# Performance work log

Hardware: AMD Instinct MI355X
Metric: run time of the kernel (lower is better)

Reference implementation:

```python
import jax, jax.numpy as jnp
import numpy as np

B, S, E, H = 2, 2048, 1024, 16
D = E // H  # head_dim = 64


def setup_inputs() -> dict:
    key = jax.random.key(0)
    ks = jax.random.split(key, 14)
    inp = {
        "query": jax.random.normal(ks[0], (B, S, E), jnp.float32),
        "key": jax.random.normal(ks[1], (B, S, E), jnp.float32),
        "value": jax.random.normal(ks[2], (B, S, E), jnp.float32),
        "adj": jax.random.normal(ks[3], (S, S), jnp.float32),
        "mask": jax.random.randint(ks[4], (B, 1, S, S), 0, 2, jnp.int32),
    }
    sc = 1.0 / np.sqrt(E)
    inp["Wq"] = jax.random.normal(ks[5], (E, E), jnp.float32) * sc
    inp["bq"] = jax.random.normal(ks[6], (E,), jnp.float32) * sc
    inp["Wk"] = jax.random.normal(ks[7], (E, E), jnp.float32) * sc
    inp["bk"] = jax.random.normal(ks[8], (E,), jnp.float32) * sc
    inp["Wv"] = jax.random.normal(ks[9], (E, E), jnp.float32) * sc
    inp["bv"] = jax.random.normal(ks[10], (E,), jnp.float32) * sc
    inp["Wo"] = jax.random.normal(ks[11], (E, E), jnp.float32) * sc
    inp["bo"] = jax.random.normal(ks[12], (E,), jnp.float32) * sc
    return inp


def reference(query, key, value, adj, mask, Wq, bq, Wk, bk, Wv, bv, Wo, bo):
    b, s, _ = query.shape
    # projections, split into heads: [B,S,E] -> [B,H,S,D]
    def heads(x, W, bias):
        y = jnp.einsum("bse,ef->bsf", x, W.T) + bias
        return y.reshape(b, s, H, D).transpose(0, 2, 1, 3)

    Q = heads(query, Wq, bq)
    K = heads(key, Wk, bk)
    V = heads(value, Wv, bv)

    # scores: [B,H,S,S], scaled by sqrt(head_dim), plus adjacency bias
    scores = jnp.einsum("bhqd,bhkd->bhqk", Q, K) / jnp.sqrt(jnp.float32(D))
    scores = scores + adj[None, None, :, :]
    scores = jnp.where(mask == 0, jnp.float32(-jnp.inf), scores)

    weights = jax.nn.softmax(scores, axis=-1)
    out = jnp.einsum("bhqk,bhkd->bhqd", weights, V)
    out = out.transpose(0, 2, 1, 3).reshape(b, s, E)
    return jnp.einsum("bse,ef->bsf", out, Wo.T) + bo
```

## Files before the change

### kernel.cpp

```cpp
#include <hip/hip_runtime.h>


typedef unsigned short ushort_t;
typedef __attribute__((ext_vector_type(8))) short bf16x8;
typedef __attribute__((ext_vector_type(4))) float floatx4;

#define NB 2
#define NS 2048
#define NE 1024
#define NH 16
#define ND 64

__device__ __forceinline__ unsigned short f2bf(float f) {
  unsigned int u = __float_as_uint(f);
  return (unsigned short)((u + 0x7fffu + ((u >> 16) & 1u)) >> 16);
}
__device__ __forceinline__ float bf2f(unsigned short h) {
  return __uint_as_float(((unsigned int)h) << 16);
}

__device__ __forceinline__ void gload_lds16(const void* g, void* l) {
  __builtin_amdgcn_global_load_lds(
      (const __attribute__((address_space(1))) unsigned int*)g,
      (__attribute__((address_space(3))) unsigned int*)l, 16, 0, 0);
}

__global__ __launch_bounds__(256) void convert_kernel(
    const float* __restrict__ q, const float* __restrict__ k, const float* __restrict__ v,
    const float* __restrict__ wq, const float* __restrict__ wk,
    const float* __restrict__ wv, const float* __restrict__ wo,
    const float* __restrict__ adj, const int* __restrict__ mask,
    ushort_t* __restrict__ qb, ushort_t* __restrict__ kb, ushort_t* __restrict__ vb,
    ushort_t* __restrict__ wqb, ushort_t* __restrict__ wkb,
    ushort_t* __restrict__ wvb, ushort_t* __restrict__ wob,
    ushort_t* __restrict__ bias)
{
  const long U1 = (long)NB * NS * NE / 8;
  const long U2 = (long)NE * NE / 8;
  long idx = (long)blockIdx.x * 256 + threadIdx.x;
  const float* src;
  ushort_t* dst;
  if (idx < U1) { src = q; dst = qb; }
  else if ((idx -= U1) < U1) { src = k; dst = kb; }
  else if ((idx -= U1) < U1) { src = v; dst = vb; }
  else if ((idx -= U1) < U2) { src = wq; dst = wqb; }
  else if ((idx -= U2) < U2) { src = wk; dst = wkb; }
  else if ((idx -= U2) < U2) { src = wv; dst = wvb; }
  else if ((idx -= U2) < U2) { src = wo; dst = wob; }
  else {
    idx -= U2;
    long flat = idx * 8;
    long rem = flat & ((1L << 22) - 1);
    const float4* a4 = (const float4*)(adj + rem);
    const int4* m4 = (const int4*)(mask + flat);
    float4 a0 = a4[0], a1 = a4[1];
    int4 m0 = m4[0], m1 = m4[1];
    const float NEGV = -1e30f;
    union { ushort_t us[8]; uint4 v4; } o;
    o.us[0] = f2bf(m0.x ? a0.x : NEGV);
    o.us[1] = f2bf(m0.y ? a0.y : NEGV);
    o.us[2] = f2bf(m0.z ? a0.z : NEGV);
    o.us[3] = f2bf(m0.w ? a0.w : NEGV);
    o.us[4] = f2bf(m1.x ? a1.x : NEGV);
    o.us[5] = f2bf(m1.y ? a1.y : NEGV);
    o.us[6] = f2bf(m1.z ? a1.z : NEGV);
    o.us[7] = f2bf(m1.w ? a1.w : NEGV);
    ((uint4*)bias)[idx] = o.v4;
    return;
  }
  const float4* s4 = (const float4*)src;
  float4 a0 = s4[idx * 2], a1 = s4[idx * 2 + 1];
  union { ushort_t us[8]; uint4 v4; } o;
  o.us[0] = f2bf(a0.x); o.us[1] = f2bf(a0.y); o.us[2] = f2bf(a0.z); o.us[3] = f2bf(a0.w);
  o.us[4] = f2bf(a1.x); o.us[5] = f2bf(a1.y); o.us[6] = f2bf(a1.z); o.us[7] = f2bf(a1.w);
  ((uint4*)dst)[idx] = o.v4;
}

__global__ __launch_bounds__(256) void qkv_kernel(
    const ushort_t* __restrict__ xq, const ushort_t* __restrict__ xk, const ushort_t* __restrict__ xv,
    const ushort_t* __restrict__ wqb, const ushort_t* __restrict__ wkb, const ushort_t* __restrict__ wvb,
    const float* __restrict__ bq, const float* __restrict__ bk, const float* __restrict__ bvv,
    ushort_t* __restrict__ Qh, ushort_t* __restrict__ Kh, ushort_t* __restrict__ Vt)
{
  __shared__ __align__(16) ushort_t As[128 * 32];
  __shared__ __align__(16) ushort_t Bs[128 * 32];

  int z = blockIdx.z;
  const ushort_t* X = (z == 0) ? xq : (z == 1) ? xk : xv;
  const ushort_t* W = (z == 0) ? wqb : (z == 1) ? wkb : wvb;
  const float* bias = (z == 0) ? bq : (z == 1) ? bk : bvv;

  int t = threadIdx.x;
  int lane = t & 63, w = t >> 6;
  int quad = lane >> 4, l16 = lane & 15;
  int wr = w >> 1, wc = w & 1;
  int m0 = blockIdx.y * 128, f0 = blockIdx.x * 128;

  floatx4 acc[4][4] = {};

  int arow = t >> 2, apart = t & 3;
  const ushort_t* Xg = X + (long)(m0 + arow) * NE + apart * 8;
  const ushort_t* Wg = W + (long)(f0 + arow) * NE + apart * 8;
  ushort_t* As_t = As + t * 8;
  ushort_t* Bs_t = Bs + t * 8;

  for (int k0 = 0; k0 < NE; k0 += 32) {
    __syncthreads();
    gload_lds16(Xg + k0, As_t);
    gload_lds16(Xg + k0 + 64 * NE, As_t + 64 * 32);
    gload_lds16(Wg + k0, Bs_t);
    gload_lds16(Wg + k0 + 64 * NE, Bs_t + 64 * 32);
    __syncthreads();
    bf16x8 af[4], bf[4];
#pragma unroll
    for (int i = 0; i < 4; i++)
      af[i] = *(const bf16x8*)(As + (wr * 64 + i * 16 + l16) * 32 + quad * 8);
#pragma unroll
    for (int j = 0; j < 4; j++)
      bf[j] = *(const bf16x8*)(Bs + (wc * 64 + j * 16 + l16) * 32 + quad * 8);
#pragma unroll
    for (int i = 0; i < 4; i++)
#pragma unroll
      for (int j = 0; j < 4; j++)
        acc[i][j] = __builtin_amdgcn_mfma_f32_16x16x32_bf16(af[i], bf[j], acc[i][j], 0, 0, 0);
  }

  ushort_t* Out = (z == 0) ? Qh : (z == 1) ? Kh : Vt;
  bool isV = (z == 2);
#pragma unroll
  for (int j = 0; j < 4; j++) {
    int f = f0 + wc * 64 + j * 16 + l16;
    float bval = bias[f];
    int h = f >> 6, d = f & 63;
#pragma unroll
    for (int i = 0; i < 4; i++) {
      int mbase = m0 + wr * 64 + i * 16 + quad * 4;
#pragma unroll
      for (int r = 0; r < 4; r++) {
        int m = mbase + r;
        int b = m >> 11, s = m & 2047;
        float y = acc[i][j][r] + bval;
        long off;
        if (!isV) off = ((long)(b * NH + h) * NS + s) * ND + d;
        else      off = ((long)(b * NH + h) * ND + d) * NS + s;
        Out[off] = f2bf(y);
      }
    }
  }
}

__global__ __launch_bounds__(256) void attn_kernel(
    const ushort_t* __restrict__ Qh, const ushort_t* __restrict__ Kh,
    const ushort_t* __restrict__ Vt, const ushort_t* __restrict__ bias,
    ushort_t* __restrict__ aout)
{
  __shared__ __align__(16) ushort_t Qs[64 * 64];
  __shared__ __align__(16) ushort_t Ks[32 * 64];
  __shared__ __align__(16) ushort_t Vts[64 * 32];
  __shared__ __align__(16) ushort_t Ps[4][16 * 32];

  int t = threadIdx.x, lane = t & 63, w = t >> 6;
  int quad = lane >> 4, l16 = lane & 15;
  int qt = blockIdx.x;
  int bh = blockIdx.y;
  int bb = bh >> 4, h = bh & 15;
  int q0 = qt * 64;

  const ushort_t* Qg = Qh + ((long)bh * NS + q0) * ND;
#pragma unroll
  for (int c = 0; c < 2; c++) {
    int idx = c * 256 + t;
    int row = idx >> 3, part = idx & 7;
    gload_lds16(Qg + (long)row * ND + part * 8, Qs + idx * 8);
  }
  __syncthreads();

  bf16x8 aq[2];
#pragma unroll
  for (int kd = 0; kd < 2; kd++)
    aq[kd] = *(const bf16x8*)(Qs + (w * 16 + l16) * 64 + kd * 32 + quad * 8);

  floatx4 acc[4] = {};
  float lsum[4] = {0.f, 0.f, 0.f, 0.f};

  const ushort_t* Kg = Kh + (long)bh * NS * ND;
  const ushort_t* Vg = Vt + (long)bh * ND * NS;
  const ushort_t* biasg = bias + (long)bb * NS * NS;

  int krow = t >> 3;
  int kc = (t & 7) ^ (krow & 7);
  int vsr = t >> 3;
  int vc = (t & 7) ^ (vsr & 7);
  int vrow = vsr * 2 + (vc >> 2);
  int vpart = vc & 3;

  const int ks_x = l16 & 7;
  const int vs_c = (((l16 & 1) * 4 + quad) ^ (l16 >> 1)) * 8;
  ushort_t* Psw = &Ps[w][0];
  const int ap_off = (l16 >> 1) * 64 + vs_c;

  for (int kt = 0; kt < NS / 32; kt++) {
    int k0 = kt * 32;
    __syncthreads();
    gload_lds16(Kg + (long)(k0 + krow) * ND + kc * 8, Ks + t * 8);
    gload_lds16(Vg + (long)vrow * NS + k0 + vpart * 8, Vts + t * 8);
    __syncthreads();

    bf16x8 bk[2][2];
#pragma unroll
    for (int jk = 0; jk < 2; jk++)
#pragma unroll
      for (int kd = 0; kd < 2; kd++)
        bk[jk][kd] = *(const bf16x8*)(Ks + (jk * 16 + l16) * 64
                                         + ((kd * 4 + quad) ^ ks_x) * 8);
    bf16x8 bv[4];
#pragma unroll
    for (int j = 0; j < 4; j++)
      bv[j] = *(const bf16x8*)(Vts + (j * 8 + (l16 >> 1)) * 64 + vs_c);

    floatx4 sc[2] = {};
#pragma unroll
    for (int jk = 0; jk < 2; jk++)
#pragma unroll
      for (int kd = 0; kd < 2; kd++)
        sc[jk] = __builtin_amdgcn_mfma_f32_16x16x32_bf16(aq[kd], bk[jk][kd], sc[jk], 0, 0, 0);

    int qg = q0 + w * 16 + quad * 4;
    float bsv[2][4];
#pragma unroll
    for (int r = 0; r < 4; r++)
#pragma unroll
      for (int jk = 0; jk < 2; jk++)
        bsv[jk][r] = bf2f(biasg[(long)(qg + r) * NS + k0 + jk * 16 + l16]);
    float p[2][4];
#pragma unroll
    for (int r = 0; r < 4; r++) {
      float s0 = sc[0][r] * 0.125f + bsv[0][r];
      float s1 = sc[1][r] * 0.125f + bsv[1][r];
      float p0 = __expf(s0);
      float p1 = __expf(s1);
      lsum[r] += p0 + p1;
      p[0][r] = p0;
      p[1][r] = p1;
    }

#pragma unroll
    for (int jk = 0; jk < 2; jk++)
#pragma unroll
      for (int r = 0; r < 4; r++) {
        int sr = quad * 2 + (r >> 1);
        int c = (r & 1) * 4 + jk * 2 + (l16 >> 3);
        Psw[sr * 64 + (c ^ sr) * 8 + (l16 & 7)] = f2bf(p[jk][r]);
      }
    asm volatile("s_waitcnt lgkmcnt(0)" ::: "memory");

    bf16x8 ap = *(const bf16x8*)(Psw + ap_off);
#pragma unroll
    for (int j = 0; j < 4; j++)
      acc[j] = __builtin_amdgcn_mfma_f32_16x16x32_bf16(ap, bv[j], acc[j], 0, 0, 0);
  }

#pragma unroll
  for (int r = 0; r < 4; r++) {
    float s = lsum[r];
    s += __shfl_xor(s, 1);
    s += __shfl_xor(s, 2);
    s += __shfl_xor(s, 4);
    s += __shfl_xor(s, 8);
    lsum[r] = s;
  }

  ushort_t* og = aout + (long)bb * NS * NE + h * ND;
#pragma unroll
  for (int r = 0; r < 4; r++) {
    int qg = q0 + w * 16 + quad * 4 + r;
    float inv = 1.0f / lsum[r];
#pragma unroll
    for (int j = 0; j < 4; j++) {
      int d = j * 16 + l16;
      og[(long)qg * NE + d] = f2bf(acc[j][r] * inv);
    }
  }
}

__global__ __launch_bounds__(256) void oproj_kernel(
    const ushort_t* __restrict__ A, const ushort_t* __restrict__ Wob,
    const float* __restrict__ bo, float* __restrict__ out)
{
  __shared__ __align__(16) ushort_t As[128 * 32];
  __shared__ __align__(16) ushort_t Bs[64 * 32];

  int t = threadIdx.x;
  int lane = t & 63, w = t >> 6;
  int quad = lane >> 4, l16 = lane & 15;
  int wr = w >> 1, wc = w & 1;
  int m0 = blockIdx.y * 128, f0 = blockIdx.x * 64;

  floatx4 acc[4][2] = {};
  int arow = t >> 2, apart = t & 3;
  const ushort_t* Xg = A + (long)(m0 + arow) * NE + apart * 8;
  const ushort_t* Wg = Wob + (long)(f0 + arow) * NE + apart * 8;
  ushort_t* As_t = As + t * 8;
  ushort_t* Bs_t = Bs + t * 8;
  bool bstage = (arow < 64);

  for (int k0 = 0; k0 < NE; k0 += 32) {
    __syncthreads();
    gload_lds16(Xg + k0, As_t);
    gload_lds16(Xg + k0 + 64 * NE, As_t + 64 * 32);
    if (bstage) gload_lds16(Wg + k0, Bs_t);
    __syncthreads();
    bf16x8 af[4], bf[2];
#pragma unroll
    for (int i = 0; i < 4; i++)
      af[i] = *(const bf16x8*)(As + (wr * 64 + i * 16 + l16) * 32 + quad * 8);
#pragma unroll
    for (int j = 0; j < 2; j++)
      bf[j] = *(const bf16x8*)(Bs + (wc * 32 + j * 16 + l16) * 32 + quad * 8);
#pragma unroll
    for (int i = 0; i < 4; i++)
#pragma unroll
      for (int j = 0; j < 2; j++)
        acc[i][j] = __builtin_amdgcn_mfma_f32_16x16x32_bf16(af[i], bf[j], acc[i][j], 0, 0, 0);
  }

#pragma unroll
  for (int j = 0; j < 2; j++) {
    int f = f0 + wc * 32 + j * 16 + l16;
    float bval = bo[f];
#pragma unroll
    for (int i = 0; i < 4; i++) {
      int mbase = m0 + wr * 64 + i * 16 + quad * 4;
#pragma unroll
      for (int r = 0; r < 4; r++) {
        int m = mbase + r;
        out[(long)m * NE + f] = acc[i][j][r] + bval;
      }
    }
  }
}

extern "C" void kernel_launch(void* const* d_in, const int* in_sizes, int n_in,
                              void* d_out, int out_size, void* d_ws, size_t ws_size,
                              hipStream_t stream) {
  const float* query = (const float*)d_in[0];
  const float* key   = (const float*)d_in[1];
  const float* value = (const float*)d_in[2];
  const float* adj   = (const float*)d_in[3];
  const int*   mask  = (const int*)d_in[4];
  const float* Wq = (const float*)d_in[5];
  const float* bq = (const float*)d_in[6];
  const float* Wk = (const float*)d_in[7];
  const float* bk = (const float*)d_in[8];
  const float* Wv = (const float*)d_in[9];
  const float* bv = (const float*)d_in[10];
  const float* Wo = (const float*)d_in[11];
  const float* bo = (const float*)d_in[12];
  float* out = (float*)d_out;

  char* ws = (char*)d_ws;
  const size_t MB = 1ull << 20;
  ushort_t* qb   = (ushort_t*)(ws + 0 * MB);
  ushort_t* kb   = (ushort_t*)(ws + 8 * MB);
  ushort_t* vb   = (ushort_t*)(ws + 16 * MB);
  ushort_t* wqb  = (ushort_t*)(ws + 24 * MB);
  ushort_t* wkb  = (ushort_t*)(ws + 26 * MB);
  ushort_t* wvb  = (ushort_t*)(ws + 28 * MB);
  ushort_t* wob  = (ushort_t*)(ws + 30 * MB);
  ushort_t* Qh   = (ushort_t*)(ws + 32 * MB);
  ushort_t* Kh   = (ushort_t*)(ws + 40 * MB);
  ushort_t* Vt   = (ushort_t*)(ws + 48 * MB);
  ushort_t* aout = (ushort_t*)(ws + 56 * MB);
  ushort_t* bias = (ushort_t*)(ws + 64 * MB);

  convert_kernel<<<12288, 256, 0, stream>>>(query, key, value, Wq, Wk, Wv, Wo,
                                            adj, mask, qb, kb, vb, wqb, wkb, wvb, wob, bias);
  qkv_kernel<<<dim3(8, 32, 3), 256, 0, stream>>>(qb, kb, vb, wqb, wkb, wvb,
                                                 bq, bk, bv, Qh, Kh, Vt);
  attn_kernel<<<dim3(32, 32), 256, 0, stream>>>(Qh, Kh, Vt, bias, aout);
  oproj_kernel<<<dim3(16, 32), 256, 0, stream>>>(aout, wob, bo, out);
}
```

Measured before the change: 316.5 us.

## Restructure attention kernel with double buffering, register P, and larger query tiles

The attention kernel now processes 128 query rows per block (32 per wave, two MFMA row groups), double-buffers K/V tiles in LDS, and prefetches the mask-bias values into registers one tile ahead. Softmax probabilities are packed with v_cvt_pk_bf16 and rearranged with permlane swaps instead of a round trip through LDS. The exponent becomes exp2, with log2e folded into the bias and scale, and blocks are remapped by a swizzled index. The aim is to hide global load latency, remove LDS traffic for P, and reuse each K/V tile across more queries. The cost is higher register pressure and half as many blocks.

```diff
diff --git a/kernel.cpp b/kernel.cpp
--- a/kernel.cpp
+++ b/kernel.cpp
@@ -4,12 +4,14 @@
 typedef unsigned short ushort_t;
 typedef __attribute__((ext_vector_type(8))) short bf16x8;
 typedef __attribute__((ext_vector_type(4))) float floatx4;
+typedef __attribute__((ext_vector_type(2))) unsigned int uintx2;
 
 #define NB 2
 #define NS 2048
 #define NE 1024
 #define NH 16
 #define ND 64
+#define LOG2E 1.44269504f
 
 __device__ __forceinline__ unsigned short f2bf(float f) {
   unsigned int u = __float_as_uint(f);
@@ -23,6 +25,37 @@
   __builtin_amdgcn_global_load_lds(
       (const __attribute__((address_space(1))) unsigned int*)g,
       (__attribute__((address_space(3))) unsigned int*)l, 16, 0, 0);
+}
+
+__device__ __forceinline__ float fexp2(float x) {
+#if __has_builtin(__builtin_amdgcn_exp2f)
+  return __builtin_amdgcn_exp2f(x);
+#else
+  return exp2f(x);
+#endif
+}
+
+__device__ __forceinline__ unsigned int cvtpk_bf16(float lo, float hi) {
+  unsigned int r;
+  asm("v_cvt_pk_bf16_f32 %0, %1, %2" : "=v"(r) : "v"(lo), "v"(hi));
+  return r;
+}
+
+__device__ __forceinline__ void pl32swap(unsigned int& a, unsigned int& b) {
+#if __has_builtin(__builtin_amdgcn_permlane32_swap)
+  uintx2 r = __builtin_amdgcn_permlane32_swap(a, b, false, false);
+  a = r[0]; b = r[1];
+#else
+  asm("v_permlane32_swap_b32 %0, %1" : "+v"(a), "+v"(b));
+#endif
+}
+__device__ __forceinline__ void pl16swap(unsigned int& a, unsigned int& b) {
+#if __has_builtin(__builtin_amdgcn_permlane16_swap)
+  uintx2 r = __builtin_amdgcn_permlane16_swap(a, b, false, false);
+  a = r[0]; b = r[1];
+#else
+  asm("v_permlane16_swap_b32 %0, %1" : "+v"(a), "+v"(b));
+#endif
 }
 
 __global__ __launch_bounds__(256) void convert_kernel(
@@ -57,14 +90,14 @@
     int4 m0 = m4[0], m1 = m4[1];
     const float NEGV = -1e30f;
     union { ushort_t us[8]; uint4 v4; } o;
-    o.us[0] = f2bf(m0.x ? a0.x : NEGV);
-    o.us[1] = f2bf(m0.y ? a0.y : NEGV);
-    o.us[2] = f2bf(m0.z ? a0.z : NEGV);
-    o.us[3] = f2bf(m0.w ? a0.w : NEGV);
-    o.us[4] = f2bf(m1.x ? a1.x : NEGV);
-    o.us[5] = f2bf(m1.y ? a1.y : NEGV);
-    o.us[6] = f2bf(m1.z ? a1.z : NEGV);
-    o.us[7] = f2bf(m1.w ? a1.w : NEGV);
+    o.us[0] = f2bf((m0.x ? a0.x : NEGV) * LOG2E);
+    o.us[1] = f2bf((m0.y ? a0.y : NEGV) * LOG2E);
+    o.us[2] = f2bf((m0.z ? a0.z : NEGV) * LOG2E);
+    o.us[3] = f2bf((m0.w ? a0.w : NEGV) * LOG2E);
+    o.us[4] = f2bf((m1.x ? a1.x : NEGV) * LOG2E);
+    o.us[5] = f2bf((m1.y ? a1.y : NEGV) * LOG2E);
+    o.us[6] = f2bf((m1.z ? a1.z : NEGV) * LOG2E);
+    o.us[7] = f2bf((m1.w ? a1.w : NEGV) * LOG2E);
     ((uint4*)bias)[idx] = o.v4;
     return;
   }
@@ -149,138 +182,159 @@
   }
 }
 
-__global__ __launch_bounds__(256) void attn_kernel(
+__global__ __launch_bounds__(256, 2) void attn_kernel(
     const ushort_t* __restrict__ Qh, const ushort_t* __restrict__ Kh,
     const ushort_t* __restrict__ Vt, const ushort_t* __restrict__ bias,
     ushort_t* __restrict__ aout)
 {
-  __shared__ __align__(16) ushort_t Qs[64 * 64];
-  __shared__ __align__(16) ushort_t Ks[32 * 64];
-  __shared__ __align__(16) ushort_t Vts[64 * 32];
-  __shared__ __align__(16) ushort_t Ps[4][16 * 32];
+  __shared__ __align__(16) ushort_t Qs[128 * 64];
+  __shared__ __align__(16) ushort_t Ks[2][32 * 64];
+  __shared__ __align__(16) ushort_t Vts[2][64 * 32];
 
   int t = threadIdx.x, lane = t & 63, w = t >> 6;
   int quad = lane >> 4, l16 = lane & 15;
-  int qt = blockIdx.x;
-  int bh = blockIdx.y;
+  int orig = blockIdx.y * 16 + blockIdx.x;
+  int wg = ((orig & 7) << 6) | (orig >> 3);
+  int qt = wg & 15, bh = wg >> 4;
   int bb = bh >> 4, h = bh & 15;
-  int q0 = qt * 64;
+  int q0 = qt * 128;
 
   const ushort_t* Qg = Qh + ((long)bh * NS + q0) * ND;
 #pragma unroll
-  for (int c = 0; c < 2; c++) {
+  for (int c = 0; c < 4; c++) {
     int idx = c * 256 + t;
-    int row = idx >> 3, part = idx & 7;
-    gload_lds16(Qg + (long)row * ND + part * 8, Qs + idx * 8);
-  }
-  __syncthreads();
-
-  bf16x8 aq[2];
-#pragma unroll
-  for (int kd = 0; kd < 2; kd++)
-    aq[kd] = *(const bf16x8*)(Qs + (w * 16 + l16) * 64 + kd * 32 + quad * 8);
-
-  floatx4 acc[4] = {};
-  float lsum[4] = {0.f, 0.f, 0.f, 0.f};
+    gload_lds16(Qg + (long)(idx >> 3) * ND + (idx & 7) * 8, Qs + idx * 8);
+  }
 
   const ushort_t* Kg = Kh + (long)bh * NS * ND;
   const ushort_t* Vg = Vt + (long)bh * ND * NS;
-  const ushort_t* biasg = bias + (long)bb * NS * NS;
-
   int krow = t >> 3;
   int kc = (t & 7) ^ (krow & 7);
   int vsr = t >> 3;
   int vc = (t & 7) ^ (vsr & 7);
   int vrow = vsr * 2 + (vc >> 2);
   int vpart = vc & 3;
+  const ushort_t* Kgp = Kg + (long)krow * ND + kc * 8;
+  const ushort_t* Vgp = Vg + (long)vrow * NS + vpart * 8;
+
+  gload_lds16(Kgp, &Ks[0][t * 8]);
+  gload_lds16(Vgp, &Vts[0][t * 8]);
+
+  const ushort_t* bg0 = bias + (long)bb * NS * NS
+                      + (long)(q0 + w * 32 + l16) * NS + quad * 4;
+  const ushort_t* bg1 = bg0 + 16 * NS;
+  uintx2 bc[2][2];
+  bc[0][0] = *(const uintx2*)bg0;
+  bc[0][1] = *(const uintx2*)(bg0 + 16);
+  bc[1][0] = *(const uintx2*)bg1;
+  bc[1][1] = *(const uintx2*)(bg1 + 16);
+
+  __syncthreads();
+
+  bf16x8 aq[2][2];
+#pragma unroll
+  for (int m = 0; m < 2; m++)
+#pragma unroll
+    for (int kd = 0; kd < 2; kd++)
+      aq[m][kd] = *(const bf16x8*)(Qs + (w * 32 + m * 16 + l16) * 64 + kd * 32 + quad * 8);
+
+  floatx4 acc[2][4] = {};
+  float lsum[2] = {0.f, 0.f};
 
   const int ks_x = l16 & 7;
   const int vs_c = (((l16 & 1) * 4 + quad) ^ (l16 >> 1)) * 8;
-  ushort_t* Psw = &Ps[w][0];
-  const int ap_off = (l16 >> 1) * 64 + vs_c;
-
+
+#pragma unroll 2
   for (int kt = 0; kt < NS / 32; kt++) {
-    int k0 = kt * 32;
+    int cur = kt & 1;
     __syncthreads();
-    gload_lds16(Kg + (long)(k0 + krow) * ND + kc * 8, Ks + t * 8);
-    gload_lds16(Vg + (long)vrow * NS + k0 + vpart * 8, Vts + t * 8);
-    __syncthreads();
-
-    bf16x8 bk[2][2];
+    if (kt < NS / 32 - 1) {
+      gload_lds16(Kgp + (long)(kt + 1) * (32 * ND), &Ks[cur ^ 1][t * 8]);
+      gload_lds16(Vgp + (kt + 1) * 32, &Vts[cur ^ 1][t * 8]);
+    }
+    uintx2 bn[2][2];
+#pragma unroll
+    for (int m = 0; m < 2; m++) { bn[m][0] = bc[m][0]; bn[m][1] = bc[m][1]; }
+    if (kt < NS / 32 - 1) {
+      bn[0][0] = *(const uintx2*)(bg0 + (kt + 1) * 32);
+      bn[0][1] = *(const uintx2*)(bg0 + (kt + 1) * 32 + 16);
+      bn[1][0] = *(const uintx2*)(bg1 + (kt + 1) * 32);
+      bn[1][1] = *(const uintx2*)(bg1 + (kt + 1) * 32 + 16);
+    }
+
+    const ushort_t* Kb = Ks[cur];
+    const ushort_t* Vb = Vts[cur];
+    bf16x8 bk[2][2], bv[4];
 #pragma unroll
     for (int jk = 0; jk < 2; jk++)
 #pragma unroll
       for (int kd = 0; kd < 2; kd++)
-        bk[jk][kd] = *(const bf16x8*)(Ks + (jk * 16 + l16) * 64
+        bk[jk][kd] = *(const bf16x8*)(Kb + (jk * 16 + l16) * 64
                                          + ((kd * 4 + quad) ^ ks_x) * 8);
-    bf16x8 bv[4];
 #pragma unroll
     for (int j = 0; j < 4; j++)
-      bv[j] = *(const bf16x8*)(Vts + (j * 8 + (l16 >> 1)) * 64 + vs_c);
-
-    floatx4 sc[2] = {};
-#pragma unroll
-    for (int jk = 0; jk < 2; jk++)
-#pragma unroll
-      for (int kd = 0; kd < 2; kd++)
-        sc[jk] = __builtin_amdgcn_mfma_f32_16x16x32_bf16(aq[kd], bk[jk][kd], sc[jk], 0, 0, 0);
-
-    int qg = q0 + w * 16 + quad * 4;
-    float bsv[2][4];
-#pragma unroll
-    for (int r = 0; r < 4; r++)
+      bv[j] = *(const bf16x8*)(Vb + (j * 8 + (l16 >> 1)) * 64 + vs_c);
+
+#pragma unroll
+    for (int m = 0; m < 2; m++) {
+      floatx4 sc[2] = {};
 #pragma unroll
       for (int jk = 0; jk < 2; jk++)
-        bsv[jk][r] = bf2f(biasg[(long)(qg + r) * NS + k0 + jk * 16 + l16]);
-    float p[2][4];
+#pragma unroll
+        for (int kd = 0; kd < 2; kd++)
+          sc[jk] = __builtin_amdgcn_mfma_f32_16x16x32_bf16(bk[jk][kd], aq[m][kd], sc[jk], 0, 0, 0);
+
+      float p[2][4];
+#pragma unroll
+      for (int jk = 0; jk < 2; jk++) {
+        unsigned int d0 = bc[m][jk][0], d1 = bc[m][jk][1];
+        float b0 = __uint_as_float(d0 << 16);
+        float b1 = __uint_as_float(d0 & 0xffff0000u);
+        float b2 = __uint_as_float(d1 << 16);
+        float b3 = __uint_as_float(d1 & 0xffff0000u);
+        p[jk][0] = fexp2(fmaf(sc[jk][0], 0.125f * LOG2E, b0));
+        p[jk][1] = fexp2(fmaf(sc[jk][1], 0.125f * LOG2E, b1));
+        p[jk][2] = fexp2(fmaf(sc[jk][2], 0.125f * LOG2E, b2));
+        p[jk][3] = fexp2(fmaf(sc[jk][3], 0.125f * LOG2E, b3));
+      }
+      lsum[m] += ((p[0][0] + p[0][1]) + (p[0][2] + p[0][3]))
+               + ((p[1][0] + p[1][1]) + (p[1][2] + p[1][3]));
+
+      unsigned int A0 = cvtpk_bf16(p[0][0], p[0][1]);
+      unsigned int A1 = cvtpk_bf16(p[0][2], p[0][3]);
+      unsigned int B0 = cvtpk_bf16(p[1][0], p[1][1]);
+      unsigned int B1 = cvtpk_bf16(p[1][2], p[1][3]);
+      pl32swap(A0, B0); pl16swap(A0, B0);
+      pl32swap(A1, B1); pl16swap(A1, B1);
+      union { unsigned int u[4]; bf16x8 v8; } pf;
+      pf.u[0] = A0; pf.u[1] = A1; pf.u[2] = B0; pf.u[3] = B1;
+#pragma unroll
+      for (int j = 0; j < 4; j++)
+        acc[m][j] = __builtin_amdgcn_mfma_f32_16x16x32_bf16(pf.v8, bv[j], acc[m][j], 0, 0, 0);
+    }
+#pragma unroll
+    for (int m = 0; m < 2; m++) { bc[m][0] = bn[m][0]; bc[m][1] = bn[m][1]; }
+  }
+
+#pragma unroll
+  for (int m = 0; m < 2; m++) {
+    float s = lsum[m];
+    s += __shfl_xor(s, 16);
+    s += __shfl_xor(s, 32);
+    lsum[m] = s;
+  }
+
+  ushort_t* og = aout + (long)bb * NS * NE + h * ND;
+#pragma unroll
+  for (int m = 0; m < 2; m++)
 #pragma unroll
     for (int r = 0; r < 4; r++) {
-      float s0 = sc[0][r] * 0.125f + bsv[0][r];
-      float s1 = sc[1][r] * 0.125f + bsv[1][r];
-      float p0 = __expf(s0);
-      float p1 = __expf(s1);
-      lsum[r] += p0 + p1;
-      p[0][r] = p0;
-      p[1][r] = p1;
-    }
-
-#pragma unroll
-    for (int jk = 0; jk < 2; jk++)
-#pragma unroll
-      for (int r = 0; r < 4; r++) {
-        int sr = quad * 2 + (r >> 1);
-        int c = (r & 1) * 4 + jk * 2 + (l16 >> 3);
-        Psw[sr * 64 + (c ^ sr) * 8 + (l16 & 7)] = f2bf(p[jk][r]);
-      }
-    asm volatile("s_waitcnt lgkmcnt(0)" ::: "memory");
-
-    bf16x8 ap = *(const bf16x8*)(Psw + ap_off);
-#pragma unroll
-    for (int j = 0; j < 4; j++)
-      acc[j] = __builtin_amdgcn_mfma_f32_16x16x32_bf16(ap, bv[j], acc[j], 0, 0, 0);
-  }
-
-#pragma unroll
-  for (int r = 0; r < 4; r++) {
-    float s = lsum[r];
-    s += __shfl_xor(s, 1);
-    s += __shfl_xor(s, 2);
-    s += __shfl_xor(s, 4);
-    s += __shfl_xor(s, 8);
-    lsum[r] = s;
-  }
-
-  ushort_t* og = aout + (long)bb * NS * NE + h * ND;
-#pragma unroll
-  for (int r = 0; r < 4; r++) {
-    int qg = q0 + w * 16 + quad * 4 + r;
-    float inv = 1.0f / lsum[r];
-#pragma unroll
-    for (int j = 0; j < 4; j++) {
-      int d = j * 16 + l16;
-      og[(long)qg * NE + d] = f2bf(acc[j][r] * inv);
-    }
-  }
+      float inv = 1.0f / __shfl(lsum[m], quad * 4 + r);
+      int qg = q0 + w * 32 + m * 16 + quad * 4 + r;
+#pragma unroll
+      for (int j = 0; j < 4; j++)
+        og[(long)qg * NE + j * 16 + l16] = f2bf(acc[m][j][r] * inv);
+    }
 }
 
 __global__ __launch_bounds__(256) void oproj_kernel(
@@ -377,6 +431,6 @@
                                             adj, mask, qb, kb, vb, wqb, wkb, wvb, wob, bias);
   qkv_kernel<<<dim3(8, 32, 3), 256, 0, stream>>>(qb, kb, vb, wqb, wkb, wvb,
                                                  bq, bk, bv, Qh, Kh, Vt);
-  attn_kernel<<<dim3(32, 32), 256, 0, stream>>>(Qh, Kh, Vt, bias, aout);
+  attn_kernel<<<dim3(16, 32), 256, 0, stream>>>(Qh, Kh, Vt, bias, aout);
   oproj_kernel<<<dim3(16, 32), 256, 0, stream>>>(aout, wob, bo, out);
 }
```

Result: no change. 313.3 us (-1.0%).
